# Performance work log

Hardware: AMD Instinct MI355X
Metric: run time of the kernel (lower is better)

Reference implementation:

```python
import jax, jax.numpy as jnp
import numpy as np
from jax.scipy.special import gammaln

B, L, D, H = 4, 2048, 512, 8
HD = D // H
SCALE = HD ** -0.5
TEMP = 1.0
PRIOR = 0.2
THRESH = 0.5
EPS = 1e-6


def setup_inputs() -> dict:
    key = jax.random.key(0)
    ks = jax.random.split(key, 6)
    xav = (6.0 / (D + D)) ** 0.5  # xavier_uniform bound for square Linear
    xav_o = (6.0 / (1 + D)) ** 0.5
    hidden = jax.random.normal(ks[0], (B, L, D), jnp.float32)
    Wq = jax.random.uniform(ks[1], (D, D), jnp.float32, -xav, xav)
    Wk = jax.random.uniform(ks[2], (D, D), jnp.float32, -xav, xav)
    Wv = jax.random.uniform(ks[3], (D, D), jnp.float32, -xav, xav)
    Wo = jax.random.uniform(ks[4], (1, D), jnp.float32, -xav_o, xav_o)
    u = jax.random.uniform(ks[5], (B, L), jnp.float32, EPS, 1.0 - EPS)
    return {"hidden": hidden, "Wq": Wq, "Wk": Wk, "Wv": Wv, "Wo": Wo, "u": u}


def _pool_one(bounds, hid):
    # bounds: [L] float (hard boundaries), hid: [L, D]
    # segment id: token belongs to the group ending at the next boundary
    ids = (jnp.cumsum(bounds) - bounds).astype(jnp.int32)  # [L]
    s = jax.ops.segment_sum(hid, ids, num_segments=L)       # [L, D]
    c = jax.ops.segment_sum(jnp.ones((L,), hid.dtype), ids, num_segments=L)
    return s / jnp.maximum(c, 1.0)[:, None]


def reference(hidden, Wq, Wk, Wv, Wo, u):
    # projections (torch Linear: y = x @ W^T)
    Q = (hidden @ Wq.T).reshape(B, L, H, HD).transpose(0, 2, 1, 3)  # [B,H,L,HD]
    K = (hidden @ Wk.T).reshape(B, L, H, HD).transpose(0, 2, 1, 3)
    V = (hidden @ Wv.T).reshape(B, L, H, HD).transpose(0, 2, 1, 3)

    scores = jnp.einsum('bhqd,bhkd->bhqk', Q, K) * SCALE            # [B,H,L,L]
    attw = jax.nn.softmax(scores, axis=-1)
    att = jnp.einsum('bhqk,bhkd->bhqd', attw, V)                    # [B,H,L,HD]
    att = att.transpose(0, 2, 1, 3).reshape(B, L, D)

    boundary_scores = attw.sum(axis=-1).mean(axis=1)                # [B,L]
    boundary_logits = (att @ Wo.T)[..., 0]                          # [B,L]

    probs = jnp.clip(jax.nn.sigmoid(boundary_logits + boundary_scores), 0.0, 1.0)
    p_logits = jnp.log(probs) - jnp.log1p(-probs)
    noise = jnp.log(u) - jnp.log1p(-u)  # logistic noise (RelaxedBernoulli rsample)
    soft = jax.nn.sigmoid((p_logits + noise) / TEMP)
    hard = (soft > THRESH).astype(soft.dtype)
    hard = hard - jax.lax.stop_gradient(soft) + soft  # straight-through

    pooled = jax.vmap(_pool_one)(hard, hidden)                      # [B,L,D]

    # Binomial(L, prior) log-prob of number of boundaries
    k = hard.sum(axis=-1)
    n = jnp.float32(L)
    logprob = (gammaln(n + 1.0) - gammaln(k + 1.0) - gammaln(n - k + 1.0)
               + k * jnp.log(jnp.float32(PRIOR)) + (n - k) * jnp.log1p(-jnp.float32(PRIOR)))
    loss = -logprob.mean() / n
    return pooled, loss
```

## Files before the change

### kernel.cpp

```cpp
#include <hip/hip_runtime.h>
#include <hip/hip_bf16.h>

#define Bsz 4
#define Lseq 2048
#define Dm 512
#define Hh 8
#define HD 64
#define QBLK 128
#define KT 64
#define KSPLIT 2
#define KHALF (Lseq / KSPLIT)
#define NTT (KHALF / KT)
#define PNT (Dm / 32)

typedef __attribute__((ext_vector_type(8))) _Float16 f16x8;
typedef __attribute__((ext_vector_type(4))) float f32x4;

__global__ void wvo_kernel(const float* __restrict__ Wv, const float* __restrict__ Wo,
                           float* __restrict__ Wvo) {
    int h = blockIdx.x >> 1;
    int c = (blockIdx.x & 1) * 256 + threadIdx.x;
    float acc = 0.f;
    #pragma unroll 8
    for (int d = 0; d < HD; ++d)
        acc += Wv[(size_t)(h * HD + d) * Dm + c] * Wo[h * HD + d];
    Wvo[h * Dm + c] = acc;
}

__device__ __forceinline__ void split8f(float4 x, float4 y, f16x8& h, f16x8& l) {
    float v[8] = {x.x, x.y, x.z, x.w, y.x, y.y, y.z, y.w};
    #pragma unroll
    for (int j = 0; j < 8; ++j) {
        _Float16 hh = (_Float16)v[j];
        h[j] = hh;
        l[j] = (_Float16)((v[j] - (float)hh) * 2048.0f);
    }
}

__global__ void __launch_bounds__(256, 2) proj_mfma_kernel(
    const float* __restrict__ A,
    const float* __restrict__ Wq, const float* __restrict__ Wk,
    _Float16* __restrict__ Qhp, _Float16* __restrict__ Qlp,
    _Float16* __restrict__ Khp, _Float16* __restrict__ Klp) {
    __shared__ _Float16 AhS[2][128][32];
    __shared__ _Float16 AlS[2][128][32];
    __shared__ _Float16 BhS[2][128][32];
    __shared__ _Float16 BlS[2][128][32];

    int tid = threadIdx.x;
    int lane = tid & 63, wid = tid >> 6;
    int wm = wid >> 1, wn = wid & 1;
    int r = lane & 15, g = lane >> 4;
    int m0 = blockIdx.x * 128;
    int nblk = blockIdx.y;
    bool isQ = nblk < 4;
    const float* Wsrc = isQ ? (Wq + (size_t)nblk * 128 * Dm)
                            : (Wk + (size_t)(nblk - 4) * 128 * Dm);
    _Float16* Hout = isQ ? Qhp : Khp;
    _Float16* Lout = isQ ? Qlp : Klp;
    int ncol0 = (nblk & 3) * 128;

    int c0 = tid * 2, c1 = tid * 2 + 1;
    int ar0 = c0 >> 2, akc0 = c0 & 3;
    int ar1 = c1 >> 2, akc1 = c1 & 3;
    int asw0 = (akc0 ^ ((ar0 >> 1) & 3)) * 8;
    int asw1 = (akc1 ^ ((ar1 >> 1) & 3)) * 8;

    const float* Abase = A + (size_t)m0 * Dm;

    float4 La0, La1, La2, La3, Lb0, Lb1, Lb2, Lb3;

#define PLOAD(T) do { \
    const float* ap0 = Abase + (size_t)ar0 * Dm + (T) * 32 + akc0 * 8; \
    const float* ap1 = Abase + (size_t)ar1 * Dm + (T) * 32 + akc1 * 8; \
    const float* bp0 = Wsrc + (size_t)ar0 * Dm + (T) * 32 + akc0 * 8; \
    const float* bp1 = Wsrc + (size_t)ar1 * Dm + (T) * 32 + akc1 * 8; \
    La0 = *(const float4*)ap0; La1 = *(const float4*)(ap0 + 4); \
    La2 = *(const float4*)ap1; La3 = *(const float4*)(ap1 + 4); \
    Lb0 = *(const float4*)bp0; Lb1 = *(const float4*)(bp0 + 4); \
    Lb2 = *(const float4*)bp1; Lb3 = *(const float4*)(bp1 + 4); \
} while (0)

#define PWRITE(BUF) do { \
    f16x8 hv, lv; \
    split8f(La0, La1, hv, lv); \
    *(f16x8*)&AhS[BUF][ar0][asw0] = hv; *(f16x8*)&AlS[BUF][ar0][asw0] = lv; \
    split8f(La2, La3, hv, lv); \
    *(f16x8*)&AhS[BUF][ar1][asw1] = hv; *(f16x8*)&AlS[BUF][ar1][asw1] = lv; \
    split8f(Lb0, Lb1, hv, lv); \
    *(f16x8*)&BhS[BUF][ar0][asw0] = hv; *(f16x8*)&BlS[BUF][ar0][asw0] = lv; \
    split8f(Lb2, Lb3, hv, lv); \
    *(f16x8*)&BhS[BUF][ar1][asw1] = hv; *(f16x8*)&BlS[BUF][ar1][asw1] = lv; \
} while (0)

    f32x4 acc1[4][4], acc2[4][4];
    #pragma unroll
    for (int mr = 0; mr < 4; ++mr)
        #pragma unroll
        for (int nr = 0; nr < 4; ++nr) {
            acc1[mr][nr] = (f32x4){0.f, 0.f, 0.f, 0.f};
            acc2[mr][nr] = (f32x4){0.f, 0.f, 0.f, 0.f};
        }

    PLOAD(0);
    PWRITE(0);
    __syncthreads();

    int sw8 = (g ^ ((r >> 1) & 3)) * 8;
    for (int t = 0; t < PNT; ++t) {
        int cur = t & 1;
        if (t + 1 < PNT) PLOAD(t + 1);
        f16x8 bhf[4], blf[4];
        #pragma unroll
        for (int nr = 0; nr < 4; ++nr) {
            int row = wn * 64 + nr * 16 + r;
            bhf[nr] = *(const f16x8*)&BhS[cur][row][sw8];
            blf[nr] = *(const f16x8*)&BlS[cur][row][sw8];
        }
        #pragma unroll
        for (int mr = 0; mr < 4; ++mr) {
            int row = wm * 64 + mr * 16 + r;
            f16x8 ah = *(const f16x8*)&AhS[cur][row][sw8];
            f16x8 al = *(const f16x8*)&AlS[cur][row][sw8];
            #pragma unroll
            for (int nr = 0; nr < 4; ++nr) {
                acc1[mr][nr] = __builtin_amdgcn_mfma_f32_16x16x32_f16(ah, bhf[nr], acc1[mr][nr], 0, 0, 0);
                acc2[mr][nr] = __builtin_amdgcn_mfma_f32_16x16x32_f16(ah, blf[nr], acc2[mr][nr], 0, 0, 0);
                acc2[mr][nr] = __builtin_amdgcn_mfma_f32_16x16x32_f16(al, bhf[nr], acc2[mr][nr], 0, 0, 0);
            }
        }
        if (t + 1 < PNT) PWRITE(cur ^ 1);
        __syncthreads();
    }

    #pragma unroll
    for (int mr = 0; mr < 4; ++mr)
        #pragma unroll
        for (int nr = 0; nr < 4; ++nr)
            #pragma unroll
            for (int j = 0; j < 4; ++j) {
                float C = acc1[mr][nr][j] + acc2[mr][nr][j] * (1.0f / 2048.0f);
                size_t m = (size_t)(m0 + wm * 64 + mr * 16 + g * 4 + j);
                size_t n = (size_t)(ncol0 + wn * 64 + nr * 16 + r);
                _Float16 hh = (_Float16)C;
                Hout[m * Dm + n] = hh;
                Lout[m * Dm + n] = (_Float16)((C - (float)hh) * 2048.0f);
            }
#undef PLOAD
#undef PWRITE
}

__global__ void vo_kernel(const float* __restrict__ hidden, const float* __restrict__ Wvo,
                          float* __restrict__ vo) {
    int bh = blockIdx.x;
    int b = bh >> 3, h = bh & 7;
    int l = blockIdx.y * 256 + threadIdx.x;
    __shared__ float w[Dm];
    for (int i = threadIdx.x; i < Dm; i += 256) w[i] = Wvo[h * Dm + i];
    __syncthreads();
    const float* hr = hidden + ((size_t)b * Lseq + l) * Dm;
    float a0 = 0.f, a1 = 0.f, a2 = 0.f, a3 = 0.f;
    #pragma unroll 8
    for (int c = 0; c < Dm; c += 4) {
        float4 v = *(const float4*)(hr + c);
        a0 += v.x * w[c]; a1 += v.y * w[c + 1]; a2 += v.z * w[c + 2]; a3 += v.w * w[c + 3];
    }
    vo[(size_t)bh * Lseq + l] = (a0 + a1) + (a2 + a3);
}

__global__ void __launch_bounds__(256, 4) attn_mfma_kernel(
    const _Float16* __restrict__ Qhp, const _Float16* __restrict__ Qlp,
    const _Float16* __restrict__ Khp, const _Float16* __restrict__ Klp,
    const float* __restrict__ vo, double* __restrict__ Yp, double* __restrict__ Zp) {
    int tid = threadIdx.x;
    int wid = tid >> 6, lane = tid & 63;
    int blk = blockIdx.x;
    int bh = blk & 31;
    int rest = blk >> 5;
    int qblk = rest & 15;
    int ks = rest >> 4;
    int b = bh >> 3, h = bh & 7;
    int q0 = qblk * QBLK + wid * 32;
    int k0 = ks * KHALF;
    int r = lane & 15, g = lane >> 4;

    __shared__ _Float16 KhS[2][KT][64];
    __shared__ _Float16 KlS[2][KT][64];
    __shared__ float vos[KHALF];

    const _Float16* Kh_g = Khp + ((size_t)(b * Lseq + k0)) * Dm + h * HD;
    const _Float16* Kl_g = Klp + ((size_t)(b * Lseq + k0)) * Dm + h * HD;

    int c0 = tid * 2, c1 = tid * 2 + 1;
    int sr0 = c0 >> 3, so0 = (c0 & 7) * 8;
    int sr1 = c1 >> 3, so1 = (c1 & 7) * 8;
    int dw0 = (so0 ^ ((sr0 & 7) << 3));
    int dw1 = (so1 ^ ((sr1 & 7) << 3));

    f16x8 nh0 = *(const f16x8*)(Kh_g + (size_t)sr0 * Dm + so0);
    f16x8 nh1 = *(const f16x8*)(Kh_g + (size_t)sr1 * Dm + so1);
    f16x8 nl0 = *(const f16x8*)(Kl_g + (size_t)sr0 * Dm + so0);
    f16x8 nl1 = *(const f16x8*)(Kl_g + (size_t)sr1 * Dm + so1);

    f16x8 Qh[2][2], Ql[2][2];
    #pragma unroll
    for (int f = 0; f < 2; ++f) {
        size_t qbase = ((size_t)(b * Lseq + q0 + f * 16 + r)) * Dm + h * HD + g * 8;
        Qh[f][0] = *(const f16x8*)(Qhp + qbase);
        Qh[f][1] = *(const f16x8*)(Qhp + qbase + 32);
        Ql[f][0] = *(const f16x8*)(Qlp + qbase);
        Ql[f][1] = *(const f16x8*)(Qlp + qbase + 32);
    }

    for (int i = tid; i < KHALF; i += 256) vos[i] = vo[(size_t)bh * Lseq + k0 + i];

    *(f16x8*)&KhS[0][sr0][dw0] = nh0;
    *(f16x8*)&KhS[0][sr1][dw1] = nh1;
    *(f16x8*)&KlS[0][sr0][dw0] = nl0;
    *(f16x8*)&KlS[0][sr1][dw1] = nl1;
    __syncthreads();

    double Yd[2] = {0.0, 0.0}, Zd[2] = {0.0, 0.0};
    int i0 = (g * 8) ^ ((r & 7) << 3);
    const float CEXP = 0.18033688011112042f;

    for (int t = 0; t < NTT; ++t) {
        int cur = t & 1;
        if (t + 1 < NTT) {
            size_t kn = (size_t)(t + 1) * KT;
            nh0 = *(const f16x8*)(Kh_g + (kn + sr0) * Dm + so0);
            nh1 = *(const f16x8*)(Kh_g + (kn + sr1) * Dm + so1);
            nl0 = *(const f16x8*)(Kl_g + (kn + sr0) * Dm + so0);
            nl1 = *(const f16x8*)(Kl_g + (kn + sr1) * Dm + so1);
        }
        float Yt[2] = {0.f, 0.f}, Zt[2] = {0.f, 0.f};
        #pragma unroll
        for (int s = 0; s < 4; ++s) {
            int row = s * 16 + r;
            f16x8 ah0 = *(const f16x8*)&KhS[cur][row][i0];
            f16x8 ah1 = *(const f16x8*)&KhS[cur][row][i0 ^ 32];
            f16x8 al0 = *(const f16x8*)&KlS[cur][row][i0];
            f16x8 al1 = *(const f16x8*)&KlS[cur][row][i0 ^ 32];
            float4 vkv = *(const float4*)&vos[t * KT + s * 16 + g * 4];
            float vk[4] = {vkv.x, vkv.y, vkv.z, vkv.w};
            #pragma unroll
            for (int f = 0; f < 2; ++f) {
                f32x4 acc1 = {0.f, 0.f, 0.f, 0.f};
                f32x4 acc2 = {0.f, 0.f, 0.f, 0.f};
                acc1 = __builtin_amdgcn_mfma_f32_16x16x32_f16(ah0, Qh[f][0], acc1, 0, 0, 0);
                acc1 = __builtin_amdgcn_mfma_f32_16x16x32_f16(ah1, Qh[f][1], acc1, 0, 0, 0);
                acc2 = __builtin_amdgcn_mfma_f32_16x16x32_f16(ah0, Ql[f][0], acc2, 0, 0, 0);
                acc2 = __builtin_amdgcn_mfma_f32_16x16x32_f16(ah1, Ql[f][1], acc2, 0, 0, 0);
                acc2 = __builtin_amdgcn_mfma_f32_16x16x32_f16(al0, Qh[f][0], acc2, 0, 0, 0);
                acc2 = __builtin_amdgcn_mfma_f32_16x16x32_f16(al1, Qh[f][1], acc2, 0, 0, 0);
                float Ych = 0.f, Zch = 0.f;
                #pragma unroll
                for (int j = 0; j < 4; ++j) {
                    float e = exp2f(fmaf(acc2[j], 1.0f / 2048.0f, acc1[j]) * CEXP);
                    Ych += e * vk[j];
                    Zch += e;
                }
                Yt[f] += Ych;
                Zt[f] += Zch;
            }
        }
        Yd[0] += (double)Yt[0]; Zd[0] += (double)Zt[0];
        Yd[1] += (double)Yt[1]; Zd[1] += (double)Zt[1];
        if (t + 1 < NTT) {
            int nxt = cur ^ 1;
            *(f16x8*)&KhS[nxt][sr0][dw0] = nh0;
            *(f16x8*)&KhS[nxt][sr1][dw1] = nh1;
            *(f16x8*)&KlS[nxt][sr0][dw0] = nl0;
            *(f16x8*)&KlS[nxt][sr1][dw1] = nl1;
        }
        __syncthreads();
    }

    #pragma unroll
    for (int f = 0; f < 2; ++f) {
        double Y = Yd[f], Z = Zd[f];
        Y += __shfl_xor(Y, 16, 64);
        Y += __shfl_xor(Y, 32, 64);
        Z += __shfl_xor(Z, 16, 64);
        Z += __shfl_xor(Z, 32, 64);
        if (lane < 16) {
            size_t idx = ((size_t)bh * Lseq + q0 + f * 16 + lane) * KSPLIT + ks;
            Yp[idx] = Y;
            Zp[idx] = Z;
        }
    }
}

__global__ void blhard_kernel(const double* __restrict__ Yp, const double* __restrict__ Zp,
                              const float* __restrict__ u, int* __restrict__ hard) {
    int i = blockIdx.x * 256 + threadIdx.x;
    int b = i >> 11, l = i & (Lseq - 1);
    float bl = 0.f;
    #pragma unroll
    for (int h = 0; h < Hh; ++h) {
        size_t base = ((size_t)(b * Hh + h) * Lseq + l) * KSPLIT;
        double Y = Yp[base] + Yp[base + 1];
        double Z = Zp[base] + Zp[base + 1];
        bl += (float)(Y / Z);
    }
    float x = bl + 1.0f;
    float probs = 1.0f / (1.0f + expf(-x));
    probs = fminf(fmaxf(probs, 0.0f), 1.0f);
    float pl = logf(probs) - log1pf(-probs);
    float un = u[i];
    float noise = logf(un) - log1pf(-un);
    float t = pl + noise;
    float soft = 1.0f / (1.0f + expf(-t));
    hard[i] = (soft > 0.5f) ? 1 : 0;
}

__global__ void scan_kernel(const int* __restrict__ hard, int* __restrict__ segstart,
                            int* __restrict__ segend, int* __restrict__ kcount) {
    int b = blockIdx.x;
    int tid = threadIdx.x;
    __shared__ int hs[Lseq];
    __shared__ int chunk[256];
    for (int i = tid; i < Lseq; i += 256) {
        segstart[b * Lseq + i] = 0;
        segend[b * Lseq + i] = 0;
    }
    int base = b * Lseq;
    int sum = 0;
    int loc[8];
    #pragma unroll
    for (int j = 0; j < 8; ++j) {
        int v = hard[base + tid * 8 + j];
        hs[tid * 8 + j] = v;
        loc[j] = sum;
        sum += v;
    }
    chunk[tid] = sum;
    __syncthreads();
    for (int off = 1; off < 256; off <<= 1) {
        int v = (tid >= off) ? chunk[tid - off] : 0;
        __syncthreads();
        chunk[tid] += v;
        __syncthreads();
    }
    int ebase = chunk[tid] - sum;
    #pragma unroll
    for (int j = 0; j < 8; ++j) {
        int ll = tid * 8 + j;
        int id = ebase + loc[j];
        if (ll == 0 || hs[ll - 1] == 1) segstart[b * Lseq + id] = ll;
        if (ll == Lseq - 1 || hs[ll] == 1) segend[b * Lseq + id] = ll + 1;
    }
    if (tid == 255) kcount[b] = chunk[255];
}

__global__ void pool_kernel(const float* __restrict__ hidden, const int* __restrict__ segstart,
                            const int* __restrict__ segend, float* __restrict__ out) {
    int i = blockIdx.x * 256 + threadIdx.x;
    int d = i & (Dm - 1);
    int s = (i >> 9) & (Lseq - 1);
    int b = i >> 20;
    int st = segstart[b * Lseq + s];
    int en = segend[b * Lseq + s];
    int n = en - st;
    float acc = 0.f;
    for (int l = st; l < en; ++l)
        acc += hidden[((size_t)b * Lseq + l) * Dm + d];
    out[i] = (n > 0) ? acc / (float)n : 0.0f;
}

__global__ void loss_kernel(const int* __restrict__ kcount, float* __restrict__ out) {
    if (threadIdx.x == 0 && blockIdx.x == 0) {
        float n = (float)Lseq;
        float acc = 0.f;
        for (int b = 0; b < Bsz; ++b) {
            float k = (float)kcount[b];
            float lp = lgammaf(n + 1.0f) - lgammaf(k + 1.0f) - lgammaf(n - k + 1.0f)
                     + k * logf(0.2f) + (n - k) * log1pf(-0.2f);
            acc += lp;
        }
        out[(size_t)Bsz * Lseq * Dm] = -(acc / (float)Bsz) / n;
    }
}

extern "C" void kernel_launch(void* const* d_in, const int* in_sizes, int n_in,
                              void* d_out, int out_size, void* d_ws, size_t ws_size,
                              hipStream_t stream) {
    const float* hidden = (const float*)d_in[0];
    const float* Wq = (const float*)d_in[1];
    const float* Wk = (const float*)d_in[2];
    const float* Wv = (const float*)d_in[3];
    const float* Wo = (const float*)d_in[4];
    const float* u  = (const float*)d_in[5];
    float* out = (float*)d_out;

    char* ws = (char*)d_ws;
    size_t off = 0;
    const size_t plane = (size_t)Bsz * Lseq * Dm * sizeof(_Float16);
    _Float16* Qhp = (_Float16*)(ws + off); off += plane;
    _Float16* Qlp = (_Float16*)(ws + off); off += plane;
    _Float16* Khp = (_Float16*)(ws + off); off += plane;
    _Float16* Klp = (_Float16*)(ws + off); off += plane;
    float* Wvo = (float*)(ws + off); off += (size_t)Hh * Dm * 4;
    float* vo = (float*)(ws + off);  off += (size_t)Bsz * Hh * Lseq * 4;
    double* Yp = (double*)(ws + off); off += (size_t)Bsz * Hh * Lseq * KSPLIT * 8;
    double* Zp = (double*)(ws + off); off += (size_t)Bsz * Hh * Lseq * KSPLIT * 8;
    int* hard = (int*)(ws + off);    off += (size_t)Bsz * Lseq * 4;
    int* segstart = (int*)(ws + off); off += (size_t)Bsz * Lseq * 4;
    int* segend = (int*)(ws + off);  off += (size_t)Bsz * Lseq * 4;
    int* kcount = (int*)(ws + off);  off += 64;

    wvo_kernel<<<dim3(16), dim3(256), 0, stream>>>(Wv, Wo, Wvo);
    proj_mfma_kernel<<<dim3((Bsz * Lseq) / 128, 8), dim3(256), 0, stream>>>(
        hidden, Wq, Wk, Qhp, Qlp, Khp, Klp);
    vo_kernel<<<dim3(Bsz * Hh, Lseq / 256), dim3(256), 0, stream>>>(hidden, Wvo, vo);
    attn_mfma_kernel<<<dim3(32 * (Lseq / QBLK) * KSPLIT), dim3(256), 0, stream>>>(
        Qhp, Qlp, Khp, Klp, vo, Yp, Zp);
    blhard_kernel<<<dim3((Bsz * Lseq) / 256), dim3(256), 0, stream>>>(Yp, Zp, u, hard);
    scan_kernel<<<dim3(Bsz), dim3(256), 0, stream>>>(hard, segstart, segend, kcount);
    pool_kernel<<<dim3((Bsz * Lseq * Dm) / 256), dim3(256), 0, stream>>>(hidden, segstart, segend, out);
    loss_kernel<<<dim3(1), dim3(64), 0, stream>>>(kcount, out);
}
```

Before: 151.9 us.

## Give each attention wave 64 query rows and split keys four ways

```diff
diff --git a/kernel.cpp b/kernel.cpp
--- a/kernel.cpp
+++ b/kernel.cpp
@@ -6,15 +6,16 @@
 #define Dm 512
 #define Hh 8
 #define HD 64
-#define QBLK 128
 #define KT 64
-#define KSPLIT 2
+#define KSPLIT 4
 #define KHALF (Lseq / KSPLIT)
 #define NTT (KHALF / KT)
 #define PNT (Dm / 32)
 
 typedef __attribute__((ext_vector_type(8))) _Float16 f16x8;
 typedef __attribute__((ext_vector_type(4))) float f32x4;
+
+#define CEXPF 0.18033688011112042f
 
 __global__ void wvo_kernel(const float* __restrict__ Wv, const float* __restrict__ Wo,
                            float* __restrict__ Wvo) {
@@ -168,7 +169,7 @@
     vo[(size_t)bh * Lseq + l] = (a0 + a1) + (a2 + a3);
 }
 
-__global__ void __launch_bounds__(256, 4) attn_mfma_kernel(
+__global__ void __launch_bounds__(256, 3) attn_mfma_kernel(
     const _Float16* __restrict__ Qhp, const _Float16* __restrict__ Qlp,
     const _Float16* __restrict__ Khp, const _Float16* __restrict__ Klp,
     const float* __restrict__ vo, double* __restrict__ Yp, double* __restrict__ Zp) {
@@ -176,11 +177,10 @@
     int wid = tid >> 6, lane = tid & 63;
     int blk = blockIdx.x;
     int bh = blk & 31;
-    int rest = blk >> 5;
-    int qblk = rest & 15;
-    int ks = rest >> 4;
+    int qblk = (blk >> 5) & 7;
+    int ks = blk >> 8;
     int b = bh >> 3, h = bh & 7;
-    int q0 = qblk * QBLK + wid * 32;
+    int q0w = qblk * 256 + wid * 64;
     int k0 = ks * KHALF;
     int r = lane & 15, g = lane >> 4;
 
@@ -202,14 +202,14 @@
     f16x8 nl0 = *(const f16x8*)(Kl_g + (size_t)sr0 * Dm + so0);
     f16x8 nl1 = *(const f16x8*)(Kl_g + (size_t)sr1 * Dm + so1);
 
-    f16x8 Qh[2][2], Ql[2][2];
-    #pragma unroll
-    for (int f = 0; f < 2; ++f) {
-        size_t qbase = ((size_t)(b * Lseq + q0 + f * 16 + r)) * Dm + h * HD + g * 8;
-        Qh[f][0] = *(const f16x8*)(Qhp + qbase);
-        Qh[f][1] = *(const f16x8*)(Qhp + qbase + 32);
-        Ql[f][0] = *(const f16x8*)(Qlp + qbase);
-        Ql[f][1] = *(const f16x8*)(Qlp + qbase + 32);
+    f16x8 QH[4][2], QL[4][2];
+    #pragma unroll
+    for (int f = 0; f < 4; ++f) {
+        size_t qbase = ((size_t)(b * Lseq + q0w + f * 16 + r)) * Dm + h * HD + g * 8;
+        QH[f][0] = *(const f16x8*)(Qhp + qbase);
+        QH[f][1] = *(const f16x8*)(Qhp + qbase + 32);
+        QL[f][0] = *(const f16x8*)(Qlp + qbase);
+        QL[f][1] = *(const f16x8*)(Qlp + qbase + 32);
     }
 
     for (int i = tid; i < KHALF; i += 256) vos[i] = vo[(size_t)bh * Lseq + k0 + i];
@@ -220,9 +220,9 @@
     *(f16x8*)&KlS[0][sr1][dw1] = nl1;
     __syncthreads();
 
-    double Yd[2] = {0.0, 0.0}, Zd[2] = {0.0, 0.0};
+    double Yd[4] = {0.0, 0.0, 0.0, 0.0};
+    double Zd[4] = {0.0, 0.0, 0.0, 0.0};
     int i0 = (g * 8) ^ ((r & 7) << 3);
-    const float CEXP = 0.18033688011112042f;
 
     for (int t = 0; t < NTT; ++t) {
         int cur = t & 1;
@@ -233,7 +233,7 @@
             nl0 = *(const f16x8*)(Kl_g + (kn + sr0) * Dm + so0);
             nl1 = *(const f16x8*)(Kl_g + (kn + sr1) * Dm + so1);
         }
-        float Yt[2] = {0.f, 0.f}, Zt[2] = {0.f, 0.f};
+        float Yt[4] = {0.f, 0.f, 0.f, 0.f}, Zt[4] = {0.f, 0.f, 0.f, 0.f};
         #pragma unroll
         for (int s = 0; s < 4; ++s) {
             int row = s * 16 + r;
@@ -244,19 +244,19 @@
             float4 vkv = *(const float4*)&vos[t * KT + s * 16 + g * 4];
             float vk[4] = {vkv.x, vkv.y, vkv.z, vkv.w};
             #pragma unroll
-            for (int f = 0; f < 2; ++f) {
-                f32x4 acc1 = {0.f, 0.f, 0.f, 0.f};
-                f32x4 acc2 = {0.f, 0.f, 0.f, 0.f};
-                acc1 = __builtin_amdgcn_mfma_f32_16x16x32_f16(ah0, Qh[f][0], acc1, 0, 0, 0);
-                acc1 = __builtin_amdgcn_mfma_f32_16x16x32_f16(ah1, Qh[f][1], acc1, 0, 0, 0);
-                acc2 = __builtin_amdgcn_mfma_f32_16x16x32_f16(ah0, Ql[f][0], acc2, 0, 0, 0);
-                acc2 = __builtin_amdgcn_mfma_f32_16x16x32_f16(ah1, Ql[f][1], acc2, 0, 0, 0);
-                acc2 = __builtin_amdgcn_mfma_f32_16x16x32_f16(al0, Qh[f][0], acc2, 0, 0, 0);
-                acc2 = __builtin_amdgcn_mfma_f32_16x16x32_f16(al1, Qh[f][1], acc2, 0, 0, 0);
+            for (int f = 0; f < 4; ++f) {
+                f32x4 a1 = {0.f, 0.f, 0.f, 0.f};
+                f32x4 a2 = {0.f, 0.f, 0.f, 0.f};
+                a1 = __builtin_amdgcn_mfma_f32_16x16x32_f16(ah0, QH[f][0], a1, 0, 0, 0);
+                a1 = __builtin_amdgcn_mfma_f32_16x16x32_f16(ah1, QH[f][1], a1, 0, 0, 0);
+                a2 = __builtin_amdgcn_mfma_f32_16x16x32_f16(ah0, QL[f][0], a2, 0, 0, 0);
+                a2 = __builtin_amdgcn_mfma_f32_16x16x32_f16(ah1, QL[f][1], a2, 0, 0, 0);
+                a2 = __builtin_amdgcn_mfma_f32_16x16x32_f16(al0, QH[f][0], a2, 0, 0, 0);
+                a2 = __builtin_amdgcn_mfma_f32_16x16x32_f16(al1, QH[f][1], a2, 0, 0, 0);
                 float Ych = 0.f, Zch = 0.f;
                 #pragma unroll
                 for (int j = 0; j < 4; ++j) {
-                    float e = exp2f(fmaf(acc2[j], 1.0f / 2048.0f, acc1[j]) * CEXP);
+                    float e = exp2f(fmaf(a2[j], 1.0f / 2048.0f, a1[j]) * CEXPF);
                     Ych += e * vk[j];
                     Zch += e;
                 }
@@ -264,8 +264,11 @@
                 Zt[f] += Zch;
             }
         }
-        Yd[0] += (double)Yt[0]; Zd[0] += (double)Zt[0];
-        Yd[1] += (double)Yt[1]; Zd[1] += (double)Zt[1];
+        #pragma unroll
+        for (int f = 0; f < 4; ++f) {
+            Yd[f] += (double)Yt[f];
+            Zd[f] += (double)Zt[f];
+        }
         if (t + 1 < NTT) {
             int nxt = cur ^ 1;
             *(f16x8*)&KhS[nxt][sr0][dw0] = nh0;
@@ -277,14 +280,14 @@
     }
 
     #pragma unroll
-    for (int f = 0; f < 2; ++f) {
+    for (int f = 0; f < 4; ++f) {
         double Y = Yd[f], Z = Zd[f];
         Y += __shfl_xor(Y, 16, 64);
         Y += __shfl_xor(Y, 32, 64);
         Z += __shfl_xor(Z, 16, 64);
         Z += __shfl_xor(Z, 32, 64);
         if (lane < 16) {
-            size_t idx = ((size_t)bh * Lseq + q0 + f * 16 + lane) * KSPLIT + ks;
+            size_t idx = ((size_t)bh * Lseq + q0w + f * 16 + lane) * KSPLIT + ks;
             Yp[idx] = Y;
             Zp[idx] = Z;
         }
@@ -299,8 +302,8 @@
     #pragma unroll
     for (int h = 0; h < Hh; ++h) {
         size_t base = ((size_t)(b * Hh + h) * Lseq + l) * KSPLIT;
-        double Y = Yp[base] + Yp[base + 1];
-        double Z = Zp[base] + Zp[base + 1];
+        double Y = (Yp[base] + Yp[base + 1]) + (Yp[base + 2] + Yp[base + 3]);
+        double Z = (Zp[base] + Zp[base + 1]) + (Zp[base + 2] + Zp[base + 3]);
         bl += (float)(Y / Z);
     }
     float x = bl + 1.0f;
@@ -413,7 +416,7 @@
     proj_mfma_kernel<<<dim3((Bsz * Lseq) / 128, 8), dim3(256), 0, stream>>>(
         hidden, Wq, Wk, Qhp, Qlp, Khp, Klp);
     vo_kernel<<<dim3(Bsz * Hh, Lseq / 256), dim3(256), 0, stream>>>(hidden, Wvo, vo);
-    attn_mfma_kernel<<<dim3(32 * (Lseq / QBLK) * KSPLIT), dim3(256), 0, stream>>>(
+    attn_mfma_kernel<<<dim3(32 * 8 * KSPLIT), dim3(256), 0, stream>>>(
         Qhp, Qlp, Khp, Klp, vo, Yp, Zp);
     blhard_kernel<<<dim3((Bsz * Lseq) / 256), dim3(256), 0, stream>>>(Yp, Zp, u, hard);
     scan_kernel<<<dim3(Bsz), dim3(256), 0, stream>>>(hard, segstart, segend, kcount);
```

Measured after the change: 177.6 us. 17.0% more time.
